# Performance work log

Hardware: AMD Instinct MI355X
Metric: run time of the kernel (lower is better)

## Reference

```python
import jax, jax.numpy as jnp
import numpy as np

SIGMA = 45.0
N, M, D = 4096, 4096, 1024


def setup_inputs() -> dict:
    key = jax.random.key(0)
    k1, k2 = jax.random.split(key)
    inputs = jax.random.normal(k1, (N, D), dtype=jnp.float32)
    samples = jax.random.normal(k2, (M, D), dtype=jnp.float32)
    return {"inputs": inputs, "samples": samples}


def _sq_dists(x, y):
    # ||x_i||^2 + ||y_j||^2 - 2 x_i.y_j  -> [N, M]
    prod = x @ y.T
    xs = jnp.sum(x * x, axis=1)[:, None]
    ys = jnp.sum(y * y, axis=1)[None, :]
    return xs + ys - 2.0 * prod


def reference(inputs, samples):
    n = inputs.shape[0]
    m = samples.shape[0]
    x = inputs.reshape(n, -1)
    y = samples.reshape(m, -1)
    inv_s2 = 1.0 / (SIGMA ** 2)

    k_xx = _sq_dists(x, x)
    k_yy = _sq_dists(y, y)
    k_xy = _sq_dists(x, y)

    # unbiased MMD: exclude diagonal terms of k_xx, k_yy
    exx = jnp.exp(-k_xx * inv_s2)
    eyy = jnp.exp(-k_yy * inv_s2)
    exy = jnp.exp(-k_xy * inv_s2)

    mmd = (jnp.sum(exx) - jnp.sum(jnp.exp(-jnp.diag(k_xx) * inv_s2))) / (n * (n - 1))
    mmd = mmd + (jnp.sum(eyy) - jnp.sum(jnp.exp(-jnp.diag(k_yy) * inv_s2))) / (m * (m - 1))
    mmd = mmd - 2.0 / (n * m) * jnp.sum(exy)
    return mmd
```

## Files before the change

kernel.cpp:

```cpp
#include <hip/hip_runtime.h>
#include <math.h>


typedef _Float16 f16_t;
typedef _Float16 f16x4 __attribute__((ext_vector_type(4)));
typedef _Float16 f16x8 __attribute__((ext_vector_type(8)));
typedef float floatx4 __attribute__((ext_vector_type(4)));

#define NROWS 4096
#define MROWS 4096
#define DDIM  1024
#define BM    128
#define BK    32
#define TILE  (BM * BK)
#define NT    (NROWS / BM)
#define TRI   (NT * (NT + 1) / 2)
#define NBLK  (2 * TRI + NT * NT)

__global__ __launch_bounds__(256) void convert_kernel(
    const float* __restrict__ X, const float* __restrict__ Y,
    f16_t* __restrict__ Xh, f16_t* __restrict__ Yh,
    float* __restrict__ nx, float* __restrict__ ny) {
    const int wid  = threadIdx.x >> 6;
    const int lane = threadIdx.x & 63;
    const int row  = blockIdx.x * 4 + wid;
    const float* src;
    f16_t* dst;
    float* nrm;
    int r;
    if (row < NROWS) {
        r = row;         src = X + (size_t)r * DDIM;
        dst = Xh + (size_t)r * DDIM;  nrm = nx;
    } else {
        r = row - NROWS; src = Y + (size_t)r * DDIM;
        dst = Yh + (size_t)r * DDIM;  nrm = ny;
    }
    const float4* s4 = (const float4*)src;
    f16x4* d4 = (f16x4*)dst;
    float s = 0.f;
    #pragma unroll
    for (int c = 0; c < 4; c++) {
        float4 v = s4[c * 64 + lane];
        f16x4 h;
        h[0] = (f16_t)v.x; h[1] = (f16_t)v.y;
        h[2] = (f16_t)v.z; h[3] = (f16_t)v.w;
        d4[c * 64 + lane] = h;
        float h0 = (float)h[0], h1 = (float)h[1];
        float h2 = (float)h[2], h3 = (float)h[3];
        s += h0 * h0 + h1 * h1 + h2 * h2 + h3 * h3;
    }
    #pragma unroll
    for (int off = 32; off > 0; off >>= 1) s += __shfl_down(s, off);
    if (lane == 0) nrm[r] = s;
}

__global__ __launch_bounds__(256) void mmd_mfma(
    const f16_t* __restrict__ Xh, const f16_t* __restrict__ Yh,
    const float* __restrict__ nx, const float* __restrict__ ny,
    double* __restrict__ partials) {
    __shared__ __align__(16) f16_t lds[2 * TILE];
    __shared__ double wred[4];

    const int b = (blockIdx.x & 7) * (NBLK / 8) + (blockIdx.x >> 3);

    const f16_t *A, *B;
    const float *nA, *nB;
    int tr, tc;
    double coef;
    if (b < 2 * TRI) {
        int u = (b < TRI) ? b : b - TRI;
        int r = 0;
        while (u >= NT - r) { u -= NT - r; r++; }
        tr = r; tc = r + u;
        double w = (tr == tc) ? 1.0 : 2.0;
        if (b < TRI) { A = Xh; B = Xh; nA = nx; nB = nx;
                       coef = w / ((double)NROWS * (double)(NROWS - 1)); }
        else         { A = Yh; B = Yh; nA = ny; nB = ny;
                       coef = w / ((double)MROWS * (double)(MROWS - 1)); }
    } else {
        int u = b - 2 * TRI;
        tr = u / NT; tc = u % NT;
        A = Xh; B = Yh; nA = nx; nB = ny;
        coef = -2.0 / ((double)NROWS * (double)MROWS);
    }

    const int t    = threadIdx.x;
    const int wave = t >> 6;
    const int lane = t & 63;
    const int wm   = wave >> 1;
    const int wn   = wave & 1;

    const f16_t* Abase = A + (size_t)tr * BM * DDIM;
    const f16_t* Bbase = B + (size_t)tc * BM * DDIM;
    const int lrow = lane >> 2;
    const int lcol = (lane & 3) * 8;
    const f16_t* gsrc[4];
    int ldsoff[4];
    #pragma unroll
    for (int i = 0; i < 4; i++) {
        int idx = wave * 4 + i;
        int tile = idx >> 3;
        int rg   = idx & 7;
        const f16_t* base = tile ? Bbase : Abase;
        gsrc[i] = base + (size_t)(rg * 16 + lrow) * DDIM + lcol;
        ldsoff[i] = tile * TILE + (rg * 16 + lrow) * BK + lcol;
    }

    const int m    = lane & 15;
    const int quad = lane >> 4;

    float na[16], nb[4];
    #pragma unroll
    for (int i = 0; i < 4; i++) {
        #pragma unroll
        for (int r = 0; r < 4; r++)
            na[i * 4 + r] = nA[tr * BM + wm * 64 + i * 16 + quad * 4 + r];
        nb[i] = nB[tc * BM + wn * 64 + i * 16 + m];
    }

    floatx4 acc_r[4][4];
    #pragma unroll
    for (int i = 0; i < 4; i++)
        #pragma unroll
        for (int j = 0; j < 4; j++) acc_r[i][j] = (floatx4){0.f, 0.f, 0.f, 0.f};

    for (int k0 = 0; k0 < DDIM; k0 += BK) {
        __syncthreads();
        #pragma unroll
        for (int i = 0; i < 4; i++) {
            __builtin_amdgcn_global_load_lds(
                (const __attribute__((address_space(1))) void*)(gsrc[i] + k0),
                (__attribute__((address_space(3))) void*)(lds + ldsoff[i]),
                16, 0, 0);
        }
        __syncthreads();

        f16x8 ah[4], bh[4];
        #pragma unroll
        for (int s = 0; s < 4; s++) {
            int arow = wm * 64 + s * 16 + m;
            int brow = wn * 64 + s * 16 + m;
            ah[s] = *(const f16x8*)&lds[arow * BK + quad * 8];
            bh[s] = *(const f16x8*)&lds[TILE + brow * BK + quad * 8];
        }
        #pragma unroll
        for (int i = 0; i < 4; i++)
            #pragma unroll
            for (int j = 0; j < 4; j++)
                acc_r[i][j] = __builtin_amdgcn_mfma_f32_16x16x32_f16(ah[i], bh[j], acc_r[i][j], 0, 0, 0);
    }

    const float inv_s2 = 1.0f / 2025.0f;
    float lsum = 0.f;
    #pragma unroll
    for (int i = 0; i < 4; i++)
        #pragma unroll
        for (int j = 0; j < 4; j++)
            #pragma unroll
            for (int r = 0; r < 4; r++) {
                float arg = (2.f * acc_r[i][j][r] - na[i * 4 + r] - nb[j]) * inv_s2;
                lsum += __expf(arg);
            }

    double d = (double)lsum;
    #pragma unroll
    for (int off = 32; off > 0; off >>= 1) d += __shfl_down(d, off);
    if (lane == 0) wred[wave] = d;
    __syncthreads();
    if (t == 0)
        partials[b] = (wred[0] + wred[1] + wred[2] + wred[3]) * coef;
}

__global__ __launch_bounds__(256) void final_reduce(const double* __restrict__ partials,
                                                    float* __restrict__ out) {
    __shared__ double red[256];
    int t = threadIdx.x;
    double s = 0.0;
    for (int i = t; i < NBLK; i += 256) s += partials[i];
    red[t] = s;
    __syncthreads();
    for (int off = 128; off > 0; off >>= 1) {
        if (t < off) red[t] += red[t + off];
        __syncthreads();
    }
    if (t == 0) {
        double mmd = red[0] - 1.0 / (double)(NROWS - 1) - 1.0 / (double)(MROWS - 1);
        out[0] = (float)mmd;
    }
}

extern "C" void kernel_launch(void* const* d_in, const int* in_sizes, int n_in,
                              void* d_out, int out_size, void* d_ws, size_t ws_size,
                              hipStream_t stream) {
    const float* X = (const float*)d_in[0];
    const float* Y = (const float*)d_in[1];
    float* out = (float*)d_out;

    char* p = (char*)d_ws;
    double* partials = (double*)p;            p += ((size_t)NBLK * sizeof(double) + 255) & ~255ULL;
    float* nx = (float*)p;                    p += (size_t)NROWS * sizeof(float);
    float* ny = (float*)p;                    p += (size_t)MROWS * sizeof(float);
    f16_t* Xh = (f16_t*)p;                    p += (size_t)NROWS * DDIM * sizeof(f16_t);
    f16_t* Yh = (f16_t*)p;

    convert_kernel<<<(NROWS + MROWS) / 4, 256, 0, stream>>>(X, Y, Xh, Yh, nx, ny);
    mmd_mfma<<<NBLK, 256, 0, stream>>>(Xh, Yh, nx, ny, partials);
    final_reduce<<<1, 256, 0, stream>>>(partials, out);
}
```

Baseline: 164.6 us.

## Add dedicated producer wave with double-buffered LDS for MFMA tile loads

Adds a fifth wave per block that only issues global-to-LDS loads into a double-buffered shared tile. The four compute waves run MFMAs on the current buffer while the next K slice is fetched. The goal is to hide global load latency that the single-buffer load/sync/compute loop left exposed. In exchange the block uses double the LDS and an extra wave that does no math, which can lower occupancy. The producer wave also holds 16 pointers and offsets in registers.

```diff
diff --git a/kernel.cpp b/kernel.cpp
--- a/kernel.cpp
+++ b/kernel.cpp
@@ -12,6 +12,7 @@
 #define DDIM  1024
 #define BM    128
 #define BK    32
+#define NIT   (DDIM / BK)
 #define TILE  (BM * BK)
 #define NT    (NROWS / BM)
 #define TRI   (NT * (NT + 1) / 2)
@@ -54,11 +55,11 @@
     if (lane == 0) nrm[r] = s;
 }
 
-__global__ __launch_bounds__(256) void mmd_mfma(
+__global__ __launch_bounds__(320) void mmd_mfma(
     const f16_t* __restrict__ Xh, const f16_t* __restrict__ Yh,
     const float* __restrict__ nx, const float* __restrict__ ny,
     double* __restrict__ partials) {
-    __shared__ __align__(16) f16_t lds[2 * TILE];
+    __shared__ __align__(16) f16_t lds[2][2 * TILE];
     __shared__ double wred[4];
 
     const int b = (blockIdx.x & 7) * (NBLK / 8) + (blockIdx.x >> 3);
@@ -87,85 +88,103 @@
     const int t    = threadIdx.x;
     const int wave = t >> 6;
     const int lane = t & 63;
+
+    const f16_t* Abase = A + (size_t)tr * BM * DDIM;
+    const f16_t* Bbase = B + (size_t)tc * BM * DDIM;
+
+    const f16_t* gsrc[16];
+    int ldsoff[16];
+    if (wave == 4) {
+        const int lrow = lane >> 2;
+        const int lcol = (lane & 3) * 8;
+        #pragma unroll
+        for (int i = 0; i < 16; i++) {
+            int tile = i >> 3;
+            int rg   = i & 7;
+            const f16_t* base = tile ? Bbase : Abase;
+            gsrc[i] = base + (size_t)(rg * 16 + lrow) * DDIM + lcol;
+            ldsoff[i] = tile * TILE + (rg * 16 + lrow) * BK + lcol;
+        }
+        #pragma unroll
+        for (int i = 0; i < 16; i++)
+            __builtin_amdgcn_global_load_lds(
+                (const __attribute__((address_space(1))) void*)gsrc[i],
+                (__attribute__((address_space(3))) void*)(&lds[0][ldsoff[i]]),
+                16, 0, 0);
+    }
+
     const int wm   = wave >> 1;
     const int wn   = wave & 1;
-
-    const f16_t* Abase = A + (size_t)tr * BM * DDIM;
-    const f16_t* Bbase = B + (size_t)tc * BM * DDIM;
-    const int lrow = lane >> 2;
-    const int lcol = (lane & 3) * 8;
-    const f16_t* gsrc[4];
-    int ldsoff[4];
-    #pragma unroll
-    for (int i = 0; i < 4; i++) {
-        int idx = wave * 4 + i;
-        int tile = idx >> 3;
-        int rg   = idx & 7;
-        const f16_t* base = tile ? Bbase : Abase;
-        gsrc[i] = base + (size_t)(rg * 16 + lrow) * DDIM + lcol;
-        ldsoff[i] = tile * TILE + (rg * 16 + lrow) * BK + lcol;
-    }
-
     const int m    = lane & 15;
     const int quad = lane >> 4;
-
     float na[16], nb[4];
-    #pragma unroll
-    for (int i = 0; i < 4; i++) {
-        #pragma unroll
-        for (int r = 0; r < 4; r++)
-            na[i * 4 + r] = nA[tr * BM + wm * 64 + i * 16 + quad * 4 + r];
-        nb[i] = nB[tc * BM + wn * 64 + i * 16 + m];
-    }
-
     floatx4 acc_r[4][4];
-    #pragma unroll
-    for (int i = 0; i < 4; i++)
-        #pragma unroll
-        for (int j = 0; j < 4; j++) acc_r[i][j] = (floatx4){0.f, 0.f, 0.f, 0.f};
-
-    for (int k0 = 0; k0 < DDIM; k0 += BK) {
-        __syncthreads();
+    if (wave < 4) {
         #pragma unroll
         for (int i = 0; i < 4; i++) {
-            __builtin_amdgcn_global_load_lds(
-                (const __attribute__((address_space(1))) void*)(gsrc[i] + k0),
-                (__attribute__((address_space(3))) void*)(lds + ldsoff[i]),
-                16, 0, 0);
+            #pragma unroll
+            for (int r = 0; r < 4; r++)
+                na[i * 4 + r] = nA[tr * BM + wm * 64 + i * 16 + quad * 4 + r];
+            nb[i] = nB[tc * BM + wn * 64 + i * 16 + m];
+        }
+        #pragma unroll
+        for (int i = 0; i < 4; i++)
+            #pragma unroll
+            for (int j = 0; j < 4; j++)
+                acc_r[i][j] = (floatx4){0.f, 0.f, 0.f, 0.f};
+    }
+
+    __syncthreads();
+
+    for (int it = 0; it < NIT; it++) {
+        if (wave == 4) {
+            if (it + 1 < NIT) {
+                const int k0 = (it + 1) * BK;
+                f16_t* dbuf = lds[(it + 1) & 1];
+                #pragma unroll
+                for (int i = 0; i < 16; i++)
+                    __builtin_amdgcn_global_load_lds(
+                        (const __attribute__((address_space(1))) void*)(gsrc[i] + k0),
+                        (__attribute__((address_space(3))) void*)(&dbuf[ldsoff[i]]),
+                        16, 0, 0);
+            }
+        } else {
+            const f16_t* cbuf = lds[it & 1];
+            f16x8 ah[4], bh[4];
+            #pragma unroll
+            for (int s = 0; s < 4; s++) {
+                int arow = wm * 64 + s * 16 + m;
+                int brow = wn * 64 + s * 16 + m;
+                ah[s] = *(const f16x8*)&cbuf[arow * BK + quad * 8];
+                bh[s] = *(const f16x8*)&cbuf[TILE + brow * BK + quad * 8];
+            }
+            #pragma unroll
+            for (int i = 0; i < 4; i++)
+                #pragma unroll
+                for (int j = 0; j < 4; j++)
+                    acc_r[i][j] = __builtin_amdgcn_mfma_f32_16x16x32_f16(
+                        ah[i], bh[j], acc_r[i][j], 0, 0, 0);
         }
         __syncthreads();
-
-        f16x8 ah[4], bh[4];
-        #pragma unroll
-        for (int s = 0; s < 4; s++) {
-            int arow = wm * 64 + s * 16 + m;
-            int brow = wn * 64 + s * 16 + m;
-            ah[s] = *(const f16x8*)&lds[arow * BK + quad * 8];
-            bh[s] = *(const f16x8*)&lds[TILE + brow * BK + quad * 8];
-        }
+    }
+
+    if (wave < 4) {
+        const float inv_s2 = 1.0f / 2025.0f;
+        float lsum = 0.f;
         #pragma unroll
         for (int i = 0; i < 4; i++)
             #pragma unroll
             for (int j = 0; j < 4; j++)
-                acc_r[i][j] = __builtin_amdgcn_mfma_f32_16x16x32_f16(ah[i], bh[j], acc_r[i][j], 0, 0, 0);
-    }
-
-    const float inv_s2 = 1.0f / 2025.0f;
-    float lsum = 0.f;
-    #pragma unroll
-    for (int i = 0; i < 4; i++)
-        #pragma unroll
-        for (int j = 0; j < 4; j++)
-            #pragma unroll
-            for (int r = 0; r < 4; r++) {
-                float arg = (2.f * acc_r[i][j][r] - na[i * 4 + r] - nb[j]) * inv_s2;
-                lsum += __expf(arg);
-            }
-
-    double d = (double)lsum;
-    #pragma unroll
-    for (int off = 32; off > 0; off >>= 1) d += __shfl_down(d, off);
-    if (lane == 0) wred[wave] = d;
+                #pragma unroll
+                for (int r = 0; r < 4; r++) {
+                    float arg = (2.f * acc_r[i][j][r] - na[i * 4 + r] - nb[j]) * inv_s2;
+                    lsum += __expf(arg);
+                }
+        double d = (double)lsum;
+        #pragma unroll
+        for (int off = 32; off > 0; off >>= 1) d += __shfl_down(d, off);
+        if (lane == 0) wred[wave] = d;
+    }
     __syncthreads();
     if (t == 0)
         partials[b] = (wred[0] + wred[1] + wred[2] + wred[3]) * coef;
@@ -204,6 +223,6 @@
     f16_t* Yh = (f16_t*)p;
 
     convert_kernel<<<(NROWS + MROWS) / 4, 256, 0, stream>>>(X, Y, Xh, Yh, nx, ny);
-    mmd_mfma<<<NBLK, 256, 0, stream>>>(Xh, Yh, nx, ny, partials);
+    mmd_mfma<<<NBLK, 320, 0, stream>>>(Xh, Yh, nx, ny, partials);
     final_reduce<<<1, 256, 0, stream>>>(partials, out);
 }
```

Measured after the change: 228.1 us. +38.6%, slower.
